# Kernel optimization log

Hardware: AMD Instinct MI355X
Metric: run time of the kernel (lower is better)

Reference implementation:

```python
import jax, jax.numpy as jnp
import numpy as np

BS = 128  # block size for weight scale blocks

def dequant_block(w, s):
    # w: [O, I] fp8-valued weights (stored fp32 here); s: [O/BS, I/BS] per-block scale_inv
    O, I = w.shape
    sf = jnp.repeat(jnp.repeat(s, BS, axis=0), BS, axis=1)[:O, :I]
    return w * sf

def setup_inputs() -> dict:
    key = jax.random.key(0)
    ks = jax.random.split(key, 7)
    T, H, F = 512, 7168, 2048
    x = jax.random.normal(ks[0], (T, H), dtype=jnp.float32)
    w_gate = jax.random.normal(ks[1], (F, H), dtype=jnp.float32)
    s_gate = jax.random.uniform(ks[2], (F // BS, H // BS), dtype=jnp.float32, minval=0.01, maxval=0.05)
    w_up = jax.random.normal(ks[3], (F, H), dtype=jnp.float32)
    s_up = jax.random.uniform(ks[4], (F // BS, H // BS), dtype=jnp.float32, minval=0.01, maxval=0.05)
    w_down = jax.random.normal(ks[5], (H, F), dtype=jnp.float32)
    s_down = jax.random.uniform(ks[6], (H // BS, F // BS), dtype=jnp.float32, minval=0.01, maxval=0.05)
    return {"x": x, "w_gate": w_gate, "s_gate": s_gate, "w_up": w_up, "s_up": s_up,
            "w_down": w_down, "s_down": s_down}

def reference(x, w_gate, s_gate, w_up, s_up, w_down, s_down):
    # SwiGLU MLP with block-dequantized FP8 weights: down(silu(gate(x)) * up(x))
    wg = dequant_block(w_gate, s_gate)   # [F, H]
    wu = dequant_block(w_up, s_up)       # [F, H]
    wd = dequant_block(w_down, s_down)   # [H, F]
    g = x @ wg.T                          # [T, F]
    u = x @ wu.T                          # [T, F]
    h = jax.nn.silu(g) * u                # [T, F]
    return h @ wd.T                       # [T, H]
```

## Files before the change

kernel.cpp:

```cpp
#include <hip/hip_runtime.h>
#include <hip/hip_bf16.h>

typedef __bf16 bf16x8_t __attribute__((ext_vector_type(8)));
typedef float f32x4_t __attribute__((ext_vector_type(4)));

#define MFMA_BF16(a, b, c) __builtin_amdgcn_mfma_f32_16x16x32_bf16((a), (b), (c), 0, 0, 0)
#define VMW(N) asm volatile("s_waitcnt vmcnt(" #N ")" ::: "memory")
#define BARRIER() __builtin_amdgcn_s_barrier()

static constexpr int T_DIM = 512;
static constexpr int H_DIM = 7168;
static constexpr int F_DIM = 2048;

__device__ __forceinline__ ushort f2bf(float f) {
    return __builtin_bit_cast(ushort, __float2bfloat16(f));
}

__device__ __forceinline__ void gload_lds16(const void* g, void* l) {
    __builtin_amdgcn_global_load_lds(
        (const __attribute__((address_space(1))) unsigned int*)g,
        (__attribute__((address_space(3))) unsigned int*)(uintptr_t)l,
        16, 0, 0);
}

__global__ void cvt_x_kernel(const float* __restrict__ in, ushort* __restrict__ outp, int n4) {
    int i = blockIdx.x * 256 + threadIdx.x;
    if (i < n4) {
        float4 v = reinterpret_cast<const float4*>(in)[i];
        ushort4 o;
        o.x = f2bf(v.x); o.y = f2bf(v.y); o.z = f2bf(v.z); o.w = f2bf(v.w);
        reinterpret_cast<ushort4*>(outp)[i] = o;
    }
}

__global__ __launch_bounds__(512, 2) void gate_up_kernel(
    const ushort* __restrict__ xb, const float* __restrict__ wg,
    const float* __restrict__ sg, const float* __restrict__ wu,
    const float* __restrict__ su, float* __restrict__ gp, int NTS, int nsplit)
{
    __shared__ ushort As[2][256 * 64];
    __shared__ float  Bs[2][128 * 64];

    const int tid = threadIdx.x;
    const int lane = tid & 63;
    const int wid = tid >> 6;
    const int wr = wid >> 1, wc = wid & 1;

    const int id = blockIdx.x;
    const int combos = nsplit << 1;
    const int c = id & (combos - 1);
    const int bn = id >> (31 - __builtin_clz(combos));
    const int bm = c & 1, bz = c >> 1;

    const int m0 = bm * 256;
    const int ks0 = bz * NTS, ks1 = ks0 + NTS;

    const float* __restrict__ Wb = (bn < 16) ? wg : wu;
    const float* __restrict__ srow = ((bn < 16) ? sg : su) + (size_t)(bn & 15) * (H_DIM / 128);
    const int nb = (bn & 15) * 128;

    f32x4_t acc[4][4] = {};

    const int a_r = tid >> 3, a_cu = tid & 7;
    const int b_r = tid >> 4, b_c32 = (tid & 15) >> 1, b_half = tid & 1;

    auto STAGE = [&](int kt, int bb) {
        const int k0 = kt * 64;
        #pragma unroll
        for (int q = 0; q < 4; ++q) {
            const int row = q * 64 + a_r;
            gload_lds16(&xb[(size_t)(m0 + row) * H_DIM + k0 + ((a_cu ^ (row & 7)) << 3)],
                        &As[bb][(q * 8192 + tid * 16) >> 1]);
        }
        #pragma unroll
        for (int q = 0; q < 4; ++q) {
            const int row = q * 32 + b_r;
            gload_lds16(&Wb[(size_t)(nb + row) * H_DIM + k0 + ((b_c32 ^ (row & 7)) << 3) + (b_half << 2)],
                        &Bs[bb][(q * 8192 + tid * 16) >> 2]);
        }
    };

    auto COMPUTE = [&](int bb) {
        #pragma unroll
        for (int ks = 0; ks < 2; ++ks) {
            const int kk = ks * 4 + (lane >> 4);
            bf16x8_t af[4];
            #pragma unroll
            for (int i = 0; i < 4; ++i) {
                const int row = wr * 64 + i * 16 + (lane & 15);
                af[i] = *reinterpret_cast<const bf16x8_t*>(&As[bb][row * 64 + ((kk ^ (row & 7)) << 3)]);
            }
            #pragma unroll
            for (int j = 0; j < 4; ++j) {
                const int row = wc * 64 + j * 16 + (lane & 15);
                const int u = kk ^ (row & 7);
                f32x4_t b0 = *reinterpret_cast<const f32x4_t*>(&Bs[bb][row * 64 + u * 8]);
                f32x4_t b1 = *reinterpret_cast<const f32x4_t*>(&Bs[bb][row * 64 + u * 8 + 4]);
                bf16x8_t bf;
                #pragma unroll
                for (int e = 0; e < 4; ++e) {
                    bf[e]     = (__bf16)b0[e];
                    bf[e + 4] = (__bf16)b1[e];
                }
                #pragma unroll
                for (int i = 0; i < 4; ++i)
                    acc[i][j] = MFMA_BF16(af[i], bf, acc[i][j]);
            }
        }
    };

    float s_cur = srow[ks0 >> 1];

    STAGE(ks0, 0);
    STAGE(ks0 + 1, 1);
    int bb = 0;
    for (int kt = ks0; kt < ks1; ++kt) {
        if (kt + 1 < ks1) { VMW(8); }
        else              { VMW(0); }
        BARRIER();
        if (((kt & 1) == 0) && kt > ks0) {
            const float s_new = srow[kt >> 1];
            const float r = s_cur / s_new;
            #pragma unroll
            for (int i = 0; i < 4; ++i)
                #pragma unroll
                for (int j = 0; j < 4; ++j)
                    acc[i][j] *= r;
            s_cur = s_new;
        }
        COMPUTE(bb);
        if (kt + 2 < ks1) {
            BARRIER();
            STAGE(kt + 2, bb);
        }
        bb ^= 1;
    }

    #pragma unroll
    for (int i = 0; i < 4; ++i)
        #pragma unroll
        for (int j = 0; j < 4; ++j)
            #pragma unroll
            for (int r = 0; r < 4; ++r) {
                const int m = m0 + wr * 64 + i * 16 + (lane >> 4) * 4 + r;
                const int nc = bn * 128 + wc * 64 + j * 16 + (lane & 15);
                gp[(size_t)bz * T_DIM * 4096 + (size_t)m * 4096 + nc] = acc[i][j][r] * s_cur;
            }
}

__global__ void h_reduce_kernel(const float* __restrict__ gp, ushort* __restrict__ hb,
                                int nsplit, int n4) {
    int i = blockIdx.x * 256 + threadIdx.x;
    if (i >= n4) return;
    const int m = i >> 9;
    const int c4 = i & 511;
    const size_t base = (size_t)m * 4096 + c4 * 4;
    const size_t stride = (size_t)T_DIM * 4096;
    float4 g = *reinterpret_cast<const float4*>(&gp[base]);
    float4 u = *reinterpret_cast<const float4*>(&gp[base + 2048]);
    for (int s = 1; s < nsplit; ++s) {
        float4 g2 = *reinterpret_cast<const float4*>(&gp[s * stride + base]);
        float4 u2 = *reinterpret_cast<const float4*>(&gp[s * stride + base + 2048]);
        g.x += g2.x; g.y += g2.y; g.z += g2.z; g.w += g2.w;
        u.x += u2.x; u.y += u2.y; u.z += u2.z; u.w += u2.w;
    }
    ushort4 o;
    o.x = f2bf(g.x / (1.0f + __expf(-g.x)) * u.x);
    o.y = f2bf(g.y / (1.0f + __expf(-g.y)) * u.y);
    o.z = f2bf(g.z / (1.0f + __expf(-g.z)) * u.z);
    o.w = f2bf(g.w / (1.0f + __expf(-g.w)) * u.w);
    reinterpret_cast<ushort4*>(hb)[i] = o;
}

template <bool DIRECT>
__global__ __launch_bounds__(512, 2) void down_kernel(
    const ushort* __restrict__ hb, const float* __restrict__ wd,
    const float* __restrict__ sd, float* __restrict__ outp, int NTS, int nsplit)
{
    __shared__ ushort As[2][256 * 64];
    __shared__ float  Bs[2][128 * 64];

    const int tid = threadIdx.x;
    const int lane = tid & 63;
    const int wid = tid >> 6;
    const int wr = wid >> 1, wc = wid & 1;

    const int id = blockIdx.x;
    const int combos = nsplit << 1;
    const int c = id & (combos - 1);
    const int bn = id >> (31 - __builtin_clz(combos));
    const int bm = c & 1, bz = c >> 1;

    const int m0 = bm * 256;
    const float* __restrict__ srow = sd + (size_t)bn * (F_DIM / 128);
    const int nb = bn * 128;
    const int ks0 = bz * NTS, ks1 = ks0 + NTS;

    f32x4_t acc[4][4] = {};

    const int a_r = tid >> 3, a_cu = tid & 7;
    const int b_r = tid >> 4, b_c32 = (tid & 15) >> 1, b_half = tid & 1;

    auto STAGE = [&](int kt, int bb) {
        const int k0 = kt * 64;
        #pragma unroll
        for (int q = 0; q < 4; ++q) {
            const int row = q * 64 + a_r;
            gload_lds16(&hb[(size_t)(m0 + row) * F_DIM + k0 + ((a_cu ^ (row & 7)) << 3)],
                        &As[bb][(q * 8192 + tid * 16) >> 1]);
        }
        #pragma unroll
        for (int q = 0; q < 4; ++q) {
            const int row = q * 32 + b_r;
            gload_lds16(&wd[(size_t)(nb + row) * F_DIM + k0 + ((b_c32 ^ (row & 7)) << 3) + (b_half << 2)],
                        &Bs[bb][(q * 8192 + tid * 16) >> 2]);
        }
    };

    auto COMPUTE = [&](int bb) {
        #pragma unroll
        for (int ks = 0; ks < 2; ++ks) {
            const int kk = ks * 4 + (lane >> 4);
            bf16x8_t af[4];
            #pragma unroll
            for (int i = 0; i < 4; ++i) {
                const int row = wr * 64 + i * 16 + (lane & 15);
                af[i] = *reinterpret_cast<const bf16x8_t*>(&As[bb][row * 64 + ((kk ^ (row & 7)) << 3)]);
            }
            #pragma unroll
            for (int j = 0; j < 4; ++j) {
                const int row = wc * 64 + j * 16 + (lane & 15);
                const int u = kk ^ (row & 7);
                f32x4_t b0 = *reinterpret_cast<const f32x4_t*>(&Bs[bb][row * 64 + u * 8]);
                f32x4_t b1 = *reinterpret_cast<const f32x4_t*>(&Bs[bb][row * 64 + u * 8 + 4]);
                bf16x8_t bf;
                #pragma unroll
                for (int e = 0; e < 4; ++e) {
                    bf[e]     = (__bf16)b0[e];
                    bf[e + 4] = (__bf16)b1[e];
                }
                #pragma unroll
                for (int i = 0; i < 4; ++i)
                    acc[i][j] = MFMA_BF16(af[i], bf, acc[i][j]);
            }
        }
    };

    float s_cur = srow[ks0 >> 1];

    STAGE(ks0, 0);
    STAGE(ks0 + 1, 1);
    int bb = 0;
    for (int kt = ks0; kt < ks1; ++kt) {
        if (kt + 1 < ks1) { VMW(8); }
        else              { VMW(0); }
        BARRIER();
        if (((kt & 1) == 0) && kt > ks0) {
            const float s_new = srow[kt >> 1];
            const float r = s_cur / s_new;
            #pragma unroll
            for (int i = 0; i < 4; ++i)
                #pragma unroll
                for (int j = 0; j < 4; ++j)
                    acc[i][j] *= r;
            s_cur = s_new;
        }
        COMPUTE(bb);
        if (kt + 2 < ks1) {
            BARRIER();
            STAGE(kt + 2, bb);
        }
        bb ^= 1;
    }

    #pragma unroll
    for (int i = 0; i < 4; ++i)
        #pragma unroll
        for (int j = 0; j < 4; ++j)
            #pragma unroll
            for (int r = 0; r < 4; ++r) {
                const int m = m0 + wr * 64 + i * 16 + (lane >> 4) * 4 + r;
                const int nc = nb + wc * 64 + j * 16 + (lane & 15);
                const float v = acc[i][j][r] * s_cur;
                if (DIRECT)
                    outp[(size_t)m * H_DIM + nc] = v;
                else
                    outp[(size_t)bz * T_DIM * H_DIM + (size_t)m * H_DIM + nc] = v;
            }
}

__global__ void d_reduce_kernel(const float* __restrict__ dp, float* __restrict__ out, int n4) {
    int i = blockIdx.x * 256 + threadIdx.x;
    if (i >= n4) return;
    const size_t stride4 = (size_t)T_DIM * H_DIM / 4;
    float4 a = reinterpret_cast<const float4*>(dp)[i];
    float4 b = reinterpret_cast<const float4*>(dp)[i + stride4];
    a.x += b.x; a.y += b.y; a.z += b.z; a.w += b.w;
    reinterpret_cast<float4*>(out)[i] = a;
}

extern "C" void kernel_launch(void* const* d_in, const int* in_sizes, int n_in,
                              void* d_out, int out_size, void* d_ws, size_t ws_size,
                              hipStream_t stream) {
    const float* x  = (const float*)d_in[0];
    const float* wg = (const float*)d_in[1];
    const float* sg = (const float*)d_in[2];
    const float* wu = (const float*)d_in[3];
    const float* su = (const float*)d_in[4];
    const float* wd = (const float*)d_in[5];
    const float* sd = (const float*)d_in[6];
    float* out = (float*)d_out;

    ushort* xb = (ushort*)d_ws;
    ushort* hb = xb + (size_t)T_DIM * H_DIM;
    float*  gp = (float*)(hb + (size_t)T_DIM * F_DIM);

    const size_t base_b = (size_t)T_DIM * H_DIM * 2 + (size_t)T_DIM * F_DIM * 2;
    const size_t split_b = (size_t)T_DIM * 4096 * 4;

    int nsplit = 1;
    if (ws_size >= base_b + 4 * split_b) nsplit = 4;
    else if (ws_size >= base_b + 2 * split_b) nsplit = 2;

    const int n4x = T_DIM * H_DIM / 4;
    cvt_x_kernel<<<n4x / 256, 256, 0, stream>>>(x, xb, n4x);

    gate_up_kernel<<<32 * 2 * nsplit, 512, 0, stream>>>(
        xb, wg, sg, wu, su, gp, (H_DIM / 64) / nsplit, nsplit);

    const int n4h = T_DIM * F_DIM / 4;
    h_reduce_kernel<<<n4h / 256, 256, 0, stream>>>(gp, hb, nsplit, n4h);

    const bool dsplit = (size_t)nsplit * split_b >= (size_t)2 * T_DIM * H_DIM * 4;
    if (dsplit) {
        float* dp = gp;
        down_kernel<false><<<56 * 2 * 2, 512, 0, stream>>>(
            hb, wd, sd, dp, (F_DIM / 64) / 2, 2);
        const int n4d = T_DIM * H_DIM / 4;
        d_reduce_kernel<<<n4d / 256, 256, 0, stream>>>(dp, out, n4d);
    } else {
        down_kernel<true><<<56 * 2 * 1, 512, 0, stream>>>(
            hb, wd, sd, out, F_DIM / 64, 1);
    }
}
```

Baseline: 99.82 us.

## Cover full M per gate/up block with K=32 tiles and deeper split-K

```diff
diff --git a/kernel.cpp b/kernel.cpp
--- a/kernel.cpp
+++ b/kernel.cpp
@@ -38,8 +38,8 @@
     const float* __restrict__ sg, const float* __restrict__ wu,
     const float* __restrict__ su, float* __restrict__ gp, int NTS, int nsplit)
 {
-    __shared__ ushort As[2][256 * 64];
-    __shared__ float  Bs[2][128 * 64];
+    __shared__ ushort As[2][512 * 32];
+    __shared__ float  Bs[2][128 * 32];
 
     const int tid = threadIdx.x;
     const int lane = tid & 63;
@@ -47,82 +47,77 @@
     const int wr = wid >> 1, wc = wid & 1;
 
     const int id = blockIdx.x;
-    const int combos = nsplit << 1;
-    const int c = id & (combos - 1);
-    const int bn = id >> (31 - __builtin_clz(combos));
-    const int bm = c & 1, bz = c >> 1;
-
-    const int m0 = bm * 256;
+    const int bz = id & (nsplit - 1);
+    const int bn = id >> (31 - __builtin_clz(nsplit));
+
     const int ks0 = bz * NTS, ks1 = ks0 + NTS;
 
     const float* __restrict__ Wb = (bn < 16) ? wg : wu;
     const float* __restrict__ srow = ((bn < 16) ? sg : su) + (size_t)(bn & 15) * (H_DIM / 128);
     const int nb = (bn & 15) * 128;
 
-    f32x4_t acc[4][4] = {};
-
-    const int a_r = tid >> 3, a_cu = tid & 7;
-    const int b_r = tid >> 4, b_c32 = (tid & 15) >> 1, b_half = tid & 1;
+    f32x4_t acc[8][4] = {};
+
+    const int a_r = tid >> 2, a_c = tid & 3;
+    const int b_r = tid >> 3, b_c16 = tid & 7;
 
     auto STAGE = [&](int kt, int bb) {
-        const int k0 = kt * 64;
+        const int k0 = kt * 32;
         #pragma unroll
         for (int q = 0; q < 4; ++q) {
-            const int row = q * 64 + a_r;
-            gload_lds16(&xb[(size_t)(m0 + row) * H_DIM + k0 + ((a_cu ^ (row & 7)) << 3)],
-                        &As[bb][(q * 8192 + tid * 16) >> 1]);
-        }
-        #pragma unroll
-        for (int q = 0; q < 4; ++q) {
-            const int row = q * 32 + b_r;
-            gload_lds16(&Wb[(size_t)(nb + row) * H_DIM + k0 + ((b_c32 ^ (row & 7)) << 3) + (b_half << 2)],
-                        &Bs[bb][(q * 8192 + tid * 16) >> 2]);
+            const int row = q * 128 + a_r;
+            gload_lds16(&xb[(size_t)row * H_DIM + k0 + ((a_c ^ (row & 3)) << 3)],
+                        &As[bb][q * 4096 + tid * 8]);
+        }
+        #pragma unroll
+        for (int q = 0; q < 2; ++q) {
+            const int row = q * 64 + b_r;
+            gload_lds16(&Wb[(size_t)(nb + row) * H_DIM + k0
+                            + (((b_c16 >> 1) ^ (row & 3)) << 3) + ((b_c16 & 1) << 2)],
+                        &Bs[bb][q * 2048 + tid * 4]);
         }
     };
 
     auto COMPUTE = [&](int bb) {
-        #pragma unroll
-        for (int ks = 0; ks < 2; ++ks) {
-            const int kk = ks * 4 + (lane >> 4);
-            bf16x8_t af[4];
-            #pragma unroll
-            for (int i = 0; i < 4; ++i) {
-                const int row = wr * 64 + i * 16 + (lane & 15);
-                af[i] = *reinterpret_cast<const bf16x8_t*>(&As[bb][row * 64 + ((kk ^ (row & 7)) << 3)]);
-            }
-            #pragma unroll
-            for (int j = 0; j < 4; ++j) {
-                const int row = wc * 64 + j * 16 + (lane & 15);
-                const int u = kk ^ (row & 7);
-                f32x4_t b0 = *reinterpret_cast<const f32x4_t*>(&Bs[bb][row * 64 + u * 8]);
-                f32x4_t b1 = *reinterpret_cast<const f32x4_t*>(&Bs[bb][row * 64 + u * 8 + 4]);
-                bf16x8_t bf;
-                #pragma unroll
-                for (int e = 0; e < 4; ++e) {
-                    bf[e]     = (__bf16)b0[e];
-                    bf[e + 4] = (__bf16)b1[e];
-                }
-                #pragma unroll
-                for (int i = 0; i < 4; ++i)
-                    acc[i][j] = MFMA_BF16(af[i], bf, acc[i][j]);
-            }
+        const int kk = lane >> 4;
+        bf16x8_t af[8];
+        #pragma unroll
+        for (int i = 0; i < 8; ++i) {
+            const int row = wr * 128 + i * 16 + (lane & 15);
+            af[i] = *reinterpret_cast<const bf16x8_t*>(&As[bb][row * 32 + ((kk ^ (row & 3)) << 3)]);
+        }
+        #pragma unroll
+        for (int j = 0; j < 4; ++j) {
+            const int row = wc * 64 + j * 16 + (lane & 15);
+            const int u = kk ^ (row & 3);
+            f32x4_t b0 = *reinterpret_cast<const f32x4_t*>(&Bs[bb][row * 32 + u * 8]);
+            f32x4_t b1 = *reinterpret_cast<const f32x4_t*>(&Bs[bb][row * 32 + u * 8 + 4]);
+            bf16x8_t bf;
+            #pragma unroll
+            for (int e = 0; e < 4; ++e) {
+                bf[e]     = (__bf16)b0[e];
+                bf[e + 4] = (__bf16)b1[e];
+            }
+            #pragma unroll
+            for (int i = 0; i < 8; ++i)
+                acc[i][j] = MFMA_BF16(af[i], bf, acc[i][j]);
         }
     };
 
-    float s_cur = srow[ks0 >> 1];
+    float s_cur = srow[ks0 >> 2];
 
     STAGE(ks0, 0);
     STAGE(ks0 + 1, 1);
     int bb = 0;
     for (int kt = ks0; kt < ks1; ++kt) {
-        if (kt + 1 < ks1) { VMW(8); }
+        if (kt + 1 < ks1) { VMW(6); }
         else              { VMW(0); }
         BARRIER();
-        if (((kt & 1) == 0) && kt > ks0) {
-            const float s_new = srow[kt >> 1];
+        if (((kt & 3) == 0) && kt > ks0) {
+            const float s_new = srow[kt >> 2];
             const float r = s_cur / s_new;
             #pragma unroll
-            for (int i = 0; i < 4; ++i)
+            for (int i = 0; i < 8; ++i)
                 #pragma unroll
                 for (int j = 0; j < 4; ++j)
                     acc[i][j] *= r;
@@ -137,12 +132,12 @@
     }
 
     #pragma unroll
-    for (int i = 0; i < 4; ++i)
+    for (int i = 0; i < 8; ++i)
         #pragma unroll
         for (int j = 0; j < 4; ++j)
             #pragma unroll
             for (int r = 0; r < 4; ++r) {
-                const int m = m0 + wr * 64 + i * 16 + (lane >> 4) * 4 + r;
+                const int m = wr * 128 + i * 16 + (lane >> 4) * 4 + r;
                 const int nc = bn * 128 + wc * 64 + j * 16 + (lane & 15);
                 gp[(size_t)bz * T_DIM * 4096 + (size_t)m * 4096 + nc] = acc[i][j][r] * s_cur;
             }
@@ -319,14 +314,15 @@
     const size_t split_b = (size_t)T_DIM * 4096 * 4;
 
     int nsplit = 1;
-    if (ws_size >= base_b + 4 * split_b) nsplit = 4;
+    if (ws_size >= base_b + 8 * split_b) nsplit = 8;
+    else if (ws_size >= base_b + 4 * split_b) nsplit = 4;
     else if (ws_size >= base_b + 2 * split_b) nsplit = 2;
 
     const int n4x = T_DIM * H_DIM / 4;
     cvt_x_kernel<<<n4x / 256, 256, 0, stream>>>(x, xb, n4x);
 
-    gate_up_kernel<<<32 * 2 * nsplit, 512, 0, stream>>>(
-        xb, wg, sg, wu, su, gp, (H_DIM / 64) / nsplit, nsplit);
+    gate_up_kernel<<<32 * nsplit, 512, 0, stream>>>(
+        xb, wg, sg, wu, su, gp, (H_DIM / 32) / nsplit, nsplit);
 
     const int n4h = T_DIM * F_DIM / 4;
     h_reduce_kernel<<<n4h / 256, 256, 0, stream>>>(gp, hb, nsplit, n4h);
```

Measured after the change: 106.1 us. 1.06x slower.
